# Kernel optimization log

Hardware: AMD Instinct MI355X
Metric: run time of the kernel (lower is better)

The kernel has to match this reference:

```python
import jax, jax.numpy as jnp
import numpy as np

B, N, F_IN, F_OUT = 8, 4096, 256, 256


def setup_inputs() -> dict:
    key = jax.random.key(0)
    k1, k2, k3 = jax.random.split(key, 3)
    H = jax.random.normal(k1, (B, N, F_IN), dtype=jnp.float32)
    W = jax.random.normal(k2, (F_IN, F_OUT), dtype=jnp.float32) * (1.0 / np.sqrt(F_IN))
    A = jax.random.normal(k3, (N, N), dtype=jnp.float32) * (1.414 * np.sqrt(2.0 / (N + N)))
    return {"H": H, "W": W, "A": A}


def reference(H, W, A):
    # HW: [B, N, F_out]
    HW = jnp.einsum('bnf,fo->bno', H, W)
    # symmetrize + relu -> nonneg adjacency [N, N]
    A_norm = jax.nn.relu((A + A.T) * 0.5)
    # degree and inverse sqrt (inf -> 0 for isolated nodes)
    D = jnp.sum(A_norm, axis=1)
    D_safe = jnp.where(D > 0, D, 1.0)
    d_inv_sqrt = jnp.where(D > 0, D_safe ** -0.5, 0.0)
    # L_norm = I - D^{-1/2} A D^{-1/2}  (diagonal scaling, no dense diag matmul)
    DAD = d_inv_sqrt[:, None] * A_norm * d_inv_sqrt[None, :]
    L_norm = jnp.eye(N, dtype=H.dtype) - DAD
    # output = relu(L_norm @ HW): [B, N, F_out]
    out = jnp.einsum('nm,bmo->bno', L_norm, HW)
    return jax.nn.relu(out)
```

## Files before the change

### kernel.cpp

```cpp
#include <hip/hip_runtime.h>
#include <stdint.h>

#define N_NODES 4096
#define F_DIM   256
#define BATCH   8

typedef __attribute__((ext_vector_type(8))) __bf16 bf16x8;
typedef __attribute__((ext_vector_type(4))) float  f32x4;
typedef __attribute__((ext_vector_type(8))) unsigned short u16x8;

typedef const __attribute__((address_space(1))) void* gas1_t;
typedef __attribute__((address_space(3))) void*       las3_t;

__device__ __forceinline__ void stage16(const void* g, void* l) {
  __builtin_amdgcn_global_load_lds((gas1_t)g, (las3_t)l, 16, 0, 0);
}

__device__ __forceinline__ unsigned short f2bf(float f) {
  union { float f; uint32_t u; } v; v.f = f;
  uint32_t u = v.u;
  return (unsigned short)((u + 0x7FFFu + ((u >> 16) & 1u)) >> 16);
}
__device__ __forceinline__ float bf2f(unsigned short u) {
  union { uint32_t u; float f; } v; v.u = ((uint32_t)u) << 16;
  return v.f;
}

__global__ __launch_bounds__(256) void k_pre(const float* __restrict__ A,
                                             unsigned short* __restrict__ Sb,
                                             float* __restrict__ D,
                                             const float4* __restrict__ H4,
                                             ushort4* __restrict__ Hb4,
                                             const float* __restrict__ W,
                                             unsigned short* __restrict__ Wt) {
  int t = threadIdx.x;
  int bid = blockIdx.y * 64 + blockIdx.x;
  {
    int i = bid * 512 + t;
    float4 v = H4[i];
    ushort4 o; o.x = f2bf(v.x); o.y = f2bf(v.y); o.z = f2bf(v.z); o.w = f2bf(v.w);
    Hb4[i] = o;
    i += 256;
    v = H4[i];
    o.x = f2bf(v.x); o.y = f2bf(v.y); o.z = f2bf(v.z); o.w = f2bf(v.w);
    Hb4[i] = o;
  }
  if (bid < 256) Wt[t * 256 + bid] = f2bf(W[bid * 256 + t]);

  int bi = blockIdx.y, bj = blockIdx.x;
  if (bj < bi) return;
  __shared__ float L1[64][65];
  __shared__ float L2[64][65];
  __shared__ float Pr[4][64];
  __shared__ float Pc[4][64];
  int i0 = bi * 64, j0 = bj * 64;
  for (int it = 0; it < 16; ++it) {
    int idx = it * 256 + t;
    int r = idx >> 6, c = idx & 63;
    L1[r][c] = A[(size_t)(i0 + r) * N_NODES + (j0 + c)];
    L2[c][r] = A[(size_t)(j0 + r) * N_NODES + (i0 + c)];
  }
  __syncthreads();
  float colsum = 0.f;
  int cfix = t & 63, q = t >> 6;
  for (int it = 0; it < 16; ++it) {
    int r = it * 4 + q;
    float v = 0.5f * (L1[r][cfix] + L2[r][cfix]);
    v = v > 0.f ? v : 0.f;
    Sb[(size_t)(i0 + r) * N_NODES + (j0 + cfix)] = f2bf(v);
    colsum += v;
    L1[r][cfix] = v;
  }
  Pc[q][cfix] = colsum;
  __syncthreads();
  {
    int r = t & 63, seg = t >> 6;
    float s = 0.f;
    for (int c = seg * 16; c < seg * 16 + 16; ++c) s += L1[r][c];
    Pr[seg][r] = s;
  }
  __syncthreads();
  if (t < 64) {
    float d = Pr[0][t] + Pr[1][t] + Pr[2][t] + Pr[3][t];
    atomicAdd(&D[i0 + t], d);
  } else if (t < 128 && bi != bj) {
    int c = t - 64;
    float d = Pc[0][c] + Pc[1][c] + Pc[2][c] + Pc[3][c];
    atomicAdd(&D[j0 + c], d);
  }
  if (bi != bj) {
    for (int it = 0; it < 16; ++it) {
      int idx = it * 256 + t;
      int ro = idx >> 6, co = idx & 63;
      Sb[(size_t)(j0 + ro) * N_NODES + (i0 + co)] = f2bf(L1[co][ro]);
    }
  }
}

__global__ void k_dinv(const float* __restrict__ D, float* __restrict__ dinv) {
  int i = blockIdx.x * blockDim.x + threadIdx.x;
  if (i < N_NODES) {
    float d = D[i];
    dinv[i] = d > 0.f ? 1.0f / sqrtf(d) : 0.f;
  }
}

__global__ __launch_bounds__(256) void k_gemm1(const unsigned short* __restrict__ Hb,
                                               const unsigned short* __restrict__ Wt,
                                               const float* __restrict__ dinv,
                                               unsigned short* __restrict__ HWb,
                                               unsigned short* __restrict__ Gt) {
  __shared__ __align__(16) unsigned short As[128 * 32];
  __shared__ __align__(16) unsigned short Bs[128 * 32];
  __shared__ __align__(16) unsigned short T[128][136];
  int t = threadIdx.x;
  int lane = t & 63;
  int q = lane >> 4, r16 = lane & 15;
  int wave = t >> 6;
  int wm = wave >> 1, wn = wave & 1;
  int m0 = blockIdx.y * 128;
  int o0 = blockIdx.x * 128;
  const int K = 256;

  const unsigned short* Abase = Hb + (size_t)m0 * K;
  const unsigned short* Bbase = Wt + (size_t)o0 * K;

  f32x4 acc[4][4];
#pragma unroll
  for (int i = 0; i < 4; ++i)
#pragma unroll
    for (int j = 0; j < 4; ++j) acc[i][j] = f32x4{0.f, 0.f, 0.f, 0.f};

  int idx0 = t, idx1 = 256 + t;
  int wb0 = (t & ~63) * 8;
  int wb1 = (256 + (t & ~63)) * 8;

  for (int kt = 0; kt < K / 32; ++kt) {
    int kof = kt * 32;
    stage16(Abase + (size_t)(idx0 >> 2) * K + kof + ((idx0 & 3) << 3), &As[wb0]);
    stage16(Abase + (size_t)(idx1 >> 2) * K + kof + ((idx1 & 3) << 3), &As[wb1]);
    stage16(Bbase + (size_t)(idx0 >> 2) * K + kof + ((idx0 & 3) << 3), &Bs[wb0]);
    stage16(Bbase + (size_t)(idx1 >> 2) * K + kof + ((idx1 & 3) << 3), &Bs[wb1]);
    __syncthreads();
    bf16x8 a[4], b[4];
#pragma unroll
    for (int mi = 0; mi < 4; ++mi)
      a[mi] = *(const bf16x8*)&As[(wm * 64 + mi * 16 + r16) * 32 + q * 8];
#pragma unroll
    for (int ni = 0; ni < 4; ++ni)
      b[ni] = *(const bf16x8*)&Bs[(wn * 64 + ni * 16 + r16) * 32 + q * 8];
#pragma unroll
    for (int mi = 0; mi < 4; ++mi)
#pragma unroll
      for (int ni = 0; ni < 4; ++ni)
        acc[mi][ni] = __builtin_amdgcn_mfma_f32_16x16x32_bf16(a[mi], b[ni], acc[mi][ni], 0, 0, 0);
    __syncthreads();
  }

#pragma unroll
  for (int mi = 0; mi < 4; ++mi) {
    int row = wm * 64 + mi * 16 + q * 4;
#pragma unroll
    for (int ni = 0; ni < 4; ++ni) {
      int col = wn * 64 + ni * 16 + r16;
#pragma unroll
      for (int rr = 0; rr < 4; ++rr) {
        unsigned short h = f2bf(acc[mi][ni][rr]);
        HWb[(size_t)(m0 + row + rr) * F_DIM + (o0 + col)] = h;
        T[col][row + rr] = h;
      }
    }
  }
  __syncthreads();
  int b = m0 >> 12, n0 = m0 & 4095;
  for (int it = 0; it < 8; ++it) {
    int unit = it * 256 + t;
    int ro = unit >> 4;
    int cs = (unit & 15) * 8;
    u16x8 v = *(const u16x8*)&T[ro][cs];
    u16x8 w;
#pragma unroll
    for (int j = 0; j < 8; ++j)
      w[j] = f2bf(bf2f(v[j]) * dinv[n0 + cs + j]);
    *(u16x8*)&Gt[(size_t)(b * 256 + o0 + ro) * N_NODES + n0 + cs] = w;
  }
}

#define LDSB 49152

__global__ __launch_bounds__(512, 2) void k_gemm2(const unsigned short* __restrict__ Sb,
                                                  const unsigned short* __restrict__ Gt,
                                                  const unsigned short* __restrict__ HWb,
                                                  const float* __restrict__ dinv,
                                                  float* __restrict__ Out) {
  __shared__ __align__(16) unsigned short LDS[3 * 24576];
  const int NT = N_NODES / 64;
  int t = threadIdx.x;
  int lane = t & 63, r16 = lane & 15, q = lane >> 4;
  int wave = t >> 6;
  int wm = wave >> 1, wn = wave & 1;

  int bid = blockIdx.x;
  int xcd = bid & 7, j = bid >> 3;
  int mt = (xcd >> 1) * 4 + (j & 3);
  int nt = (xcd & 1) * 8 + (j >> 2);
  int m0 = mt * 256, n0 = nt * 128;

  const char* aSrc[4]; const char* bSrc[2];
  uint32_t aDst[4], bDst[2];
#pragma unroll
  for (int i = 0; i < 4; ++i) {
    int slot = i * 512 + t;
    int row = slot >> 3;
    int c = (slot & 7) ^ (row & 7);
    aSrc[i] = (const char*)Sb + (size_t)(m0 + row) * 8192 + c * 16;
    aDst[i] = (uint32_t)(i * 512 + (t & ~63)) * 16;
  }
#pragma unroll
  for (int i = 0; i < 2; ++i) {
    int slot = i * 512 + t;
    int row = slot >> 3;
    int c = (slot & 7) ^ (row & 7);
    bSrc[i] = (const char*)Gt + (size_t)(n0 + row) * 8192 + c * 16;
    bDst[i] = 32768u + (uint32_t)(i * 512 + (t & ~63)) * 16;
  }

  int aoff[4][2], boff[4][2];
#pragma unroll
  for (int mi = 0; mi < 4; ++mi) {
    int ra = wm * 64 + mi * 16 + r16;
#pragma unroll
    for (int ks = 0; ks < 2; ++ks)
      aoff[mi][ks] = ra * 128 + (((ks * 4 + q) ^ (ra & 7)) << 4);
  }
#pragma unroll
  for (int ni = 0; ni < 4; ++ni) {
    int rb = wn * 64 + ni * 16 + r16;
#pragma unroll
    for (int ks = 0; ks < 2; ++ks)
      boff[ni][ks] = 32768 + rb * 128 + (((ks * 4 + q) ^ (rb & 7)) << 4);
  }

  f32x4 acc[4][4];
#pragma unroll
  for (int i = 0; i < 4; ++i)
#pragma unroll
    for (int jj = 0; jj < 4; ++jj) acc[i][jj] = f32x4{0.f, 0.f, 0.f, 0.f};

  auto stage_tile = [&](int kt2, uint32_t bufByte) {
    size_t kb = (size_t)kt2 * 128;
#pragma unroll
    for (int i = 0; i < 4; ++i)
      stage16(aSrc[i] + kb, (char*)LDS + bufByte + aDst[i]);
#pragma unroll
    for (int i = 0; i < 2; ++i)
      stage16(bSrc[i] + kb, (char*)LDS + bufByte + bDst[i]);
  };

  auto tile_body = [&](int kt, uint32_t cur, int mode) {
    bf16x8 aR[4][2], bR[4][2];
#pragma unroll
    for (int mi = 0; mi < 4; ++mi)
#pragma unroll
      for (int ks = 0; ks < 2; ++ks)
        aR[mi][ks] = *(const bf16x8*)((const char*)LDS + cur + aoff[mi][ks]);
#pragma unroll
    for (int ni = 0; ni < 4; ++ni)
#pragma unroll
      for (int ks = 0; ks < 2; ++ks)
        bR[ni][ks] = *(const bf16x8*)((const char*)LDS + cur + boff[ni][ks]);
    if (mode == 2) {
      uint32_t stg = cur + 2 * LDSB;
      if (stg >= 3 * LDSB) stg -= 3 * LDSB;
      stage_tile(kt + 2, stg);
    }
    __builtin_amdgcn_sched_barrier(0);
    __builtin_amdgcn_s_setprio(1);
#pragma unroll
    for (int ks = 0; ks < 2; ++ks)
#pragma unroll
      for (int mi = 0; mi < 4; ++mi)
#pragma unroll
        for (int ni = 0; ni < 4; ++ni)
          acc[mi][ni] = __builtin_amdgcn_mfma_f32_16x16x32_bf16(aR[mi][ks], bR[ni][ks], acc[mi][ni], 0, 0, 0);
    __builtin_amdgcn_s_setprio(0);
    if (mode == 2) {
      asm volatile("s_waitcnt vmcnt(6)" ::: "memory");
    } else if (mode == 1) {
      asm volatile("s_waitcnt vmcnt(0)" ::: "memory");
    }
    if (mode != 0) {
      __builtin_amdgcn_s_barrier();
      __builtin_amdgcn_sched_barrier(0);
    }
  };

  stage_tile(0, 0);
  stage_tile(1, LDSB);
  asm volatile("s_waitcnt vmcnt(6)" ::: "memory");
  __builtin_amdgcn_s_barrier();
  __builtin_amdgcn_sched_barrier(0);

  uint32_t cur = 0;
#pragma unroll 1
  for (int kt = 0; kt < NT - 2; ++kt) {
    tile_body(kt, cur, 2);
    cur += LDSB; if (cur == 3 * LDSB) cur = 0;
  }
  tile_body(NT - 2, cur, 1);
  cur += LDSB; if (cur == 3 * LDSB) cur = 0;
  tile_body(NT - 1, cur, 0);

  int bq = n0 >> 8;
#pragma unroll
  for (int mi = 0; mi < 4; ++mi) {
    int row = m0 + wm * 64 + mi * 16 + q * 4;
    float di[4];
#pragma unroll
    for (int rr = 0; rr < 4; ++rr) di[rr] = dinv[row + rr];
#pragma unroll
    for (int ni = 0; ni < 4; ++ni) {
      int col = n0 + wn * 64 + ni * 16 + r16;
      int o = col & 255;
#pragma unroll
      for (int rr = 0; rr < 4; ++rr) {
        size_t oi = ((size_t)bq * N_NODES + (row + rr)) * F_DIM + o;
        float u = bf2f(HWb[oi]) - di[rr] * acc[mi][ni][rr];
        Out[oi] = u > 0.f ? u : 0.f;
      }
    }
  }
}

extern "C" void kernel_launch(void* const* d_in, const int* in_sizes, int n_in,
                              void* d_out, int out_size, void* d_ws, size_t ws_size,
                              hipStream_t stream) {
  (void)in_sizes; (void)n_in; (void)out_size; (void)ws_size;
  const float* H = (const float*)d_in[0];
  const float* W = (const float*)d_in[1];
  const float* A = (const float*)d_in[2];
  float* out = (float*)d_out;

  char* ws = (char*)d_ws;
  size_t off = 0;
  auto alloc = [&](size_t bytes) {
    char* p = ws + off;
    off += (bytes + 255) & ~(size_t)255;
    return p;
  };
  float*          Dd   = (float*)alloc((size_t)N_NODES * 4);
  float*          dinv = (float*)alloc((size_t)N_NODES * 4);
  unsigned short* Sb   = (unsigned short*)alloc((size_t)N_NODES * N_NODES * 2);
  unsigned short* HWb  = (unsigned short*)alloc((size_t)BATCH * N_NODES * F_DIM * 2);
  unsigned short* Gt   = (unsigned short*)alloc((size_t)BATCH * F_DIM * N_NODES * 2);
  unsigned short* Wt   = (unsigned short*)alloc((size_t)F_DIM * F_DIM * 2);
  unsigned short* Hb   = (unsigned short*)alloc((size_t)BATCH * N_NODES * F_DIM * 2);

  hipMemsetAsync(Dd, 0, N_NODES * 4, stream);
  k_pre<<<dim3(64, 64), 256, 0, stream>>>(A, Sb, Dd, (const float4*)H, (ushort4*)Hb, W, Wt);
  k_dinv<<<16, 256, 0, stream>>>(Dd, dinv);
  k_gemm1<<<dim3(2, 256), 256, 0, stream>>>(Hb, Wt, dinv, HWb, Gt);
  k_gemm2<<<dim3(256), 512, 0, stream>>>(Sb, Gt, HWb, dinv, out);
}
```

Baseline: 216.9 us.

## Vectorize adjacency preprocessing and stage full-K GEMM1 tiles with swizzled LDS

The adjacency preprocessing now uses float4 global loads, and both the row-major and transposed bf16 stores of the symmetrized matrix become 16-byte vector writes instead of scalar ones. GEMM1 moves to 512 threads and loads the whole K=256 slice of both operands into 128 KB of XOR-swizzled LDS in one pass, removing the per-K-step barriers. The dinv scaling loads are vectorized. The large LDS footprint limits occupancy to one block per CU, and the whole-tile load forgoes overlap between loading and MFMA work.

```diff
diff --git a/kernel.cpp b/kernel.cpp
--- a/kernel.cpp
+++ b/kernel.cpp
@@ -49,50 +49,73 @@
 
   int bi = blockIdx.y, bj = blockIdx.x;
   if (bj < bi) return;
-  __shared__ float L1[64][65];
-  __shared__ float L2[64][65];
-  __shared__ float Pr[4][64];
+
+  __shared__ __align__(16) float T1[64][68];
+  __shared__ float Tt[64][67];
+  __shared__ float Pr4[64][4];
   __shared__ float Pc[4][64];
   int i0 = bi * 64, j0 = bj * 64;
-  for (int it = 0; it < 16; ++it) {
+
+#pragma unroll
+  for (int it = 0; it < 4; ++it) {
     int idx = it * 256 + t;
-    int r = idx >> 6, c = idx & 63;
-    L1[r][c] = A[(size_t)(i0 + r) * N_NODES + (j0 + c)];
-    L2[c][r] = A[(size_t)(j0 + r) * N_NODES + (i0 + c)];
-  }
-  __syncthreads();
-  float colsum = 0.f;
-  int cfix = t & 63, q = t >> 6;
-  for (int it = 0; it < 16; ++it) {
-    int r = it * 4 + q;
-    float v = 0.5f * (L1[r][cfix] + L2[r][cfix]);
-    v = v > 0.f ? v : 0.f;
-    Sb[(size_t)(i0 + r) * N_NODES + (j0 + cfix)] = f2bf(v);
-    colsum += v;
-    L1[r][cfix] = v;
-  }
-  Pc[q][cfix] = colsum;
-  __syncthreads();
+    int r = idx >> 4, c4 = (idx & 15) * 4;
+    float4 v1 = *(const float4*)(A + (size_t)(i0 + r) * N_NODES + j0 + c4);
+    *(float4*)&T1[r][c4] = v1;
+    float4 v2 = *(const float4*)(A + (size_t)(j0 + r) * N_NODES + i0 + c4);
+    Tt[c4 + 0][r] = v2.x; Tt[c4 + 1][r] = v2.y; Tt[c4 + 2][r] = v2.z; Tt[c4 + 3][r] = v2.w;
+  }
+  __syncthreads();
+
   {
-    int r = t & 63, seg = t >> 6;
+    int r = t >> 2, cb = (t & 3) * 8;
+    float rowpart = 0.f;
+#pragma unroll
+    for (int g = 0; g < 2; ++g) {
+      int c0 = cb + g * 32;
+      u16x8 u;
+      float vv[8];
+#pragma unroll
+      for (int i = 0; i < 8; ++i) {
+        float v = 0.5f * (T1[r][c0 + i] + Tt[r][c0 + i]);
+        v = v > 0.f ? v : 0.f;
+        vv[i] = v;
+        rowpart += v;
+        u[i] = f2bf(v);
+      }
+      *(u16x8*)&Sb[(size_t)(i0 + r) * N_NODES + j0 + c0] = u;
+      *(float4*)&T1[r][c0]     = make_float4(vv[0], vv[1], vv[2], vv[3]);
+      *(float4*)&T1[r][c0 + 4] = make_float4(vv[4], vv[5], vv[6], vv[7]);
+    }
+    Pr4[r][t & 3] = rowpart;
+  }
+  __syncthreads();
+
+  {
+    int c = t & 63, seg = t >> 6;
     float s = 0.f;
-    for (int c = seg * 16; c < seg * 16 + 16; ++c) s += L1[r][c];
-    Pr[seg][r] = s;
-  }
-  __syncthreads();
+#pragma unroll
+    for (int i = 0; i < 16; ++i) s += T1[seg * 16 + i][c];
+    Pc[seg][c] = s;
+  }
+  __syncthreads();
+
   if (t < 64) {
-    float d = Pr[0][t] + Pr[1][t] + Pr[2][t] + Pr[3][t];
-    atomicAdd(&D[i0 + t], d);
+    atomicAdd(&D[i0 + t], Pr4[t][0] + Pr4[t][1] + Pr4[t][2] + Pr4[t][3]);
   } else if (t < 128 && bi != bj) {
     int c = t - 64;
-    float d = Pc[0][c] + Pc[1][c] + Pc[2][c] + Pc[3][c];
-    atomicAdd(&D[j0 + c], d);
-  }
+    atomicAdd(&D[j0 + c], Pc[0][c] + Pc[1][c] + Pc[2][c] + Pc[3][c]);
+  }
+
   if (bi != bj) {
-    for (int it = 0; it < 16; ++it) {
-      int idx = it * 256 + t;
-      int ro = idx >> 6, co = idx & 63;
-      Sb[(size_t)(j0 + ro) * N_NODES + (i0 + co)] = f2bf(L1[co][ro]);
+#pragma unroll
+    for (int it = 0; it < 2; ++it) {
+      int u = it * 256 + t;
+      int co = u >> 3, rc = (u & 7) * 8;
+      u16x8 o;
+#pragma unroll
+      for (int i = 0; i < 8; ++i) o[i] = f2bf(T1[rc + i][co]);
+      *(u16x8*)&Sb[(size_t)(j0 + co) * N_NODES + i0 + rc] = o;
     }
   }
 }
@@ -105,84 +128,93 @@
   }
 }
 
-__global__ __launch_bounds__(256) void k_gemm1(const unsigned short* __restrict__ Hb,
+__global__ __launch_bounds__(512) void k_gemm1(const unsigned short* __restrict__ Hb,
                                                const unsigned short* __restrict__ Wt,
                                                const float* __restrict__ dinv,
                                                unsigned short* __restrict__ HWb,
                                                unsigned short* __restrict__ Gt) {
-  __shared__ __align__(16) unsigned short As[128 * 32];
-  __shared__ __align__(16) unsigned short Bs[128 * 32];
-  __shared__ __align__(16) unsigned short T[128][136];
+  __shared__ __align__(16) unsigned short L[65536];
   int t = threadIdx.x;
-  int lane = t & 63;
-  int q = lane >> 4, r16 = lane & 15;
+  int lane = t & 63, r16 = lane & 15, q = lane >> 4;
   int wave = t >> 6;
-  int wm = wave >> 1, wn = wave & 1;
+  int wm = wave >> 2, wn = wave & 3;
+  int nh = blockIdx.x;
   int m0 = blockIdx.y * 128;
-  int o0 = blockIdx.x * 128;
-  const int K = 256;
-
-  const unsigned short* Abase = Hb + (size_t)m0 * K;
-  const unsigned short* Bbase = Wt + (size_t)o0 * K;
-
-  f32x4 acc[4][4];
+  int n0 = nh * 128;
+
+#pragma unroll
+  for (int i = 0; i < 8; ++i) {
+    int s = i * 512 + t;
+    int row = s >> 5, cl = s & 31;
+    int cs = cl ^ (row & 7);
+    uint32_t dst = (uint32_t)(i * 512 + (t & ~63)) * 16;
+    stage16(Hb + (size_t)(m0 + row) * 256 + cs * 8, (char*)L + dst);
+    stage16(Wt + (size_t)(n0 + row) * 256 + cs * 8, (char*)L + 65536 + dst);
+  }
+  __syncthreads();
+
+  f32x4 acc[4][2];
 #pragma unroll
   for (int i = 0; i < 4; ++i)
 #pragma unroll
-    for (int j = 0; j < 4; ++j) acc[i][j] = f32x4{0.f, 0.f, 0.f, 0.f};
-
-  int idx0 = t, idx1 = 256 + t;
-  int wb0 = (t & ~63) * 8;
-  int wb1 = (256 + (t & ~63)) * 8;
-
-  for (int kt = 0; kt < K / 32; ++kt) {
-    int kof = kt * 32;
-    stage16(Abase + (size_t)(idx0 >> 2) * K + kof + ((idx0 & 3) << 3), &As[wb0]);
-    stage16(Abase + (size_t)(idx1 >> 2) * K + kof + ((idx1 & 3) << 3), &As[wb1]);
-    stage16(Bbase + (size_t)(idx0 >> 2) * K + kof + ((idx0 & 3) << 3), &Bs[wb0]);
-    stage16(Bbase + (size_t)(idx1 >> 2) * K + kof + ((idx1 & 3) << 3), &Bs[wb1]);
-    __syncthreads();
-    bf16x8 a[4], b[4];
+    for (int j = 0; j < 2; ++j) acc[i][j] = f32x4{0.f, 0.f, 0.f, 0.f};
+
+#pragma unroll
+  for (int ks = 0; ks < 8; ++ks) {
+    bf16x8 a[4], b[2];
+#pragma unroll
+    for (int mi = 0; mi < 4; ++mi) {
+      int ra = wm * 64 + mi * 16 + r16;
+      a[mi] = *(const bf16x8*)((const char*)L + ra * 512 + (((ks * 4 + q) ^ (ra & 7)) << 4));
+    }
+#pragma unroll
+    for (int ni = 0; ni < 2; ++ni) {
+      int rb = wn * 32 + ni * 16 + r16;
+      b[ni] = *(const bf16x8*)((const char*)L + 65536 + rb * 512 + (((ks * 4 + q) ^ (rb & 7)) << 4));
+    }
 #pragma unroll
     for (int mi = 0; mi < 4; ++mi)
-      a[mi] = *(const bf16x8*)&As[(wm * 64 + mi * 16 + r16) * 32 + q * 8];
-#pragma unroll
-    for (int ni = 0; ni < 4; ++ni)
-      b[ni] = *(const bf16x8*)&Bs[(wn * 64 + ni * 16 + r16) * 32 + q * 8];
-#pragma unroll
-    for (int mi = 0; mi < 4; ++mi)
-#pragma unroll
-      for (int ni = 0; ni < 4; ++ni)
+#pragma unroll
+      for (int ni = 0; ni < 2; ++ni)
         acc[mi][ni] = __builtin_amdgcn_mfma_f32_16x16x32_bf16(a[mi], b[ni], acc[mi][ni], 0, 0, 0);
-    __syncthreads();
-  }
-
+  }
+  __syncthreads();
+
+  unsigned short (*T)[136] = (unsigned short (*)[136])L;
 #pragma unroll
   for (int mi = 0; mi < 4; ++mi) {
-    int row = wm * 64 + mi * 16 + q * 4;
-#pragma unroll
-    for (int ni = 0; ni < 4; ++ni) {
-      int col = wn * 64 + ni * 16 + r16;
+    int rowl = wm * 64 + mi * 16 + q * 4;
+#pragma unroll
+    for (int ni = 0; ni < 2; ++ni) {
+      int coll = wn * 32 + ni * 16 + r16;
 #pragma unroll
       for (int rr = 0; rr < 4; ++rr) {
         unsigned short h = f2bf(acc[mi][ni][rr]);
-        HWb[(size_t)(m0 + row + rr) * F_DIM + (o0 + col)] = h;
-        T[col][row + rr] = h;
+        HWb[(size_t)(m0 + rowl + rr) * F_DIM + (n0 + coll)] = h;
+        T[coll][rowl + rr] = h;
       }
     }
   }
   __syncthreads();
-  int b = m0 >> 12, n0 = m0 & 4095;
-  for (int it = 0; it < 8; ++it) {
-    int unit = it * 256 + t;
-    int ro = unit >> 4;
-    int cs = (unit & 15) * 8;
-    u16x8 v = *(const u16x8*)&T[ro][cs];
+
+  int b = m0 >> 12, nb = m0 & 4095;
+#pragma unroll
+  for (int i = 0; i < 4; ++i) {
+    int u = i * 512 + t;
+    int co = u >> 4, cs = (u & 15) * 8;
+    u16x8 v = *(const u16x8*)&T[co][cs];
+    float4 d0 = *(const float4*)&dinv[nb + cs];
+    float4 d1 = *(const float4*)&dinv[nb + cs + 4];
     u16x8 w;
-#pragma unroll
-    for (int j = 0; j < 8; ++j)
-      w[j] = f2bf(bf2f(v[j]) * dinv[n0 + cs + j]);
-    *(u16x8*)&Gt[(size_t)(b * 256 + o0 + ro) * N_NODES + n0 + cs] = w;
+    w[0] = f2bf(bf2f(v[0]) * d0.x);
+    w[1] = f2bf(bf2f(v[1]) * d0.y);
+    w[2] = f2bf(bf2f(v[2]) * d0.z);
+    w[3] = f2bf(bf2f(v[3]) * d0.w);
+    w[4] = f2bf(bf2f(v[4]) * d1.x);
+    w[5] = f2bf(bf2f(v[5]) * d1.y);
+    w[6] = f2bf(bf2f(v[6]) * d1.z);
+    w[7] = f2bf(bf2f(v[7]) * d1.w);
+    *(u16x8*)&Gt[(size_t)(b * 256 + n0 + co) * N_NODES + nb + cs] = w;
   }
 }
 
@@ -359,6 +391,6 @@
   hipMemsetAsync(Dd, 0, N_NODES * 4, stream);
   k_pre<<<dim3(64, 64), 256, 0, stream>>>(A, Sb, Dd, (const float4*)H, (ushort4*)Hb, W, Wt);
   k_dinv<<<16, 256, 0, stream>>>(Dd, dinv);
-  k_gemm1<<<dim3(2, 256), 256, 0, stream>>>(Hb, Wt, dinv, HWb, Gt);
+  k_gemm1<<<dim3(2, 256), 512, 0, stream>>>(Hb, Wt, dinv, HWb, Gt);
   k_gemm2<<<dim3(256), 512, 0, stream>>>(Sb, Gt, HWb, dinv, out);
 }
```

Result: no change. 220.1 us (+1.5%).
